# Performance work log

Hardware: AMD Instinct MI355X
Metric: run time of the kernel (lower is better)

The kernel has to match this reference:

```python
import jax, jax.numpy as jnp
import numpy as np
import math

NUM_HEADS = 16
HEAD_DIM = 128
HIDDEN = 2048
ROPE_THETA = 10000.0


def rotate_half(x):
    half = x.shape[-1] // 2
    return jnp.concatenate((-x[..., half:], x[..., :half]), axis=-1)


def rope_cos_sin(seq_len, dtype):
    # rotary_dim == head_dim (even)
    inv_freq = 1.0 / (ROPE_THETA ** (jnp.arange(0, HEAD_DIM, 2, dtype=jnp.float32) / HEAD_DIM))
    pos = jnp.arange(seq_len, dtype=jnp.float32)
    freqs = pos[:, None] * inv_freq[None, :]          # [S, HEAD_DIM/2]
    emb = jnp.concatenate((freqs, freqs), axis=-1)    # [S, HEAD_DIM]
    return jnp.cos(emb).astype(dtype), jnp.sin(emb).astype(dtype)


def setup_inputs() -> dict:
    key = jax.random.key(0)
    ks = jax.random.split(key, 5)
    B, S = 2, 2048
    scale = 1.0 / math.sqrt(HIDDEN)
    return {
        "hidden_states": jax.random.normal(ks[0], (B, S, HIDDEN), dtype=jnp.float32),
        "Wq": jax.random.normal(ks[1], (NUM_HEADS * HEAD_DIM, HIDDEN), dtype=jnp.float32) * scale,
        "Wk": jax.random.normal(ks[2], (NUM_HEADS * HEAD_DIM, HIDDEN), dtype=jnp.float32) * scale,
        "Wv": jax.random.normal(ks[3], (NUM_HEADS * HEAD_DIM, HIDDEN), dtype=jnp.float32) * scale,
        "Wo": jax.random.normal(ks[4], (HIDDEN, NUM_HEADS * HEAD_DIM), dtype=jnp.float32) * scale,
        "attention_mask": jnp.ones((B, S), dtype=bool),
    }


def reference(hidden_states, Wq, Wk, Wv, Wo, attention_mask):
    B, S, _ = hidden_states.shape
    # projections (Linear with weight [out, in]): y = x @ W.T
    def proj(W):
        y = jnp.einsum('bsh,oh->bso', hidden_states, W)
        return y.reshape(B, S, NUM_HEADS, HEAD_DIM).transpose(0, 2, 1, 3)  # [B,H,S,D]
    q, k, v = proj(Wq), proj(Wk), proj(Wv)

    cos, sin = rope_cos_sin(S, q.dtype)               # [S, D]
    cos = cos[None, None]                             # [1,1,S,D]
    sin = sin[None, None]
    q = q * cos + rotate_half(q) * sin
    k = k * cos + rotate_half(k) * sin

    scores = jnp.einsum('bhqd,bhkd->bhqk', q, k) / math.sqrt(HEAD_DIM)
    neg = jnp.finfo(scores.dtype).min
    causal = jnp.tril(jnp.ones((S, S), dtype=bool))   # past_len = 0
    scores = jnp.where(causal[None, None], scores, neg)
    key_mask = attention_mask[:, None, None, :]       # [B,1,1,S] bool
    scores = jnp.where(key_mask, scores, neg)

    attn = jax.nn.softmax(scores.astype(jnp.float32), axis=-1).astype(q.dtype)
    out = jnp.einsum('bhqk,bhkd->bhqd', attn, v)
    out = out.transpose(0, 2, 1, 3).reshape(B, S, NUM_HEADS * HEAD_DIM)
    return jnp.einsum('bso,ho->bsh', out, Wo)
```

## Files before the change

kernel.cpp:

```cpp
#include <hip/hip_runtime.h>
#include <stdint.h>

typedef unsigned short ushort_t;
typedef __attribute__((ext_vector_type(8))) __bf16 bf16x8;
typedef __attribute__((ext_vector_type(4))) float f32x4;

#define HIDDEN 2048
#define NHEADS 16
#define HDIM 128
#define SEQ 2048
#define BATCH 2
#define MROWS (BATCH*SEQ)

#define AS1 __attribute__((address_space(1)))
#define AS3 __attribute__((address_space(3)))

__device__ __forceinline__ ushort_t f2bf(float f) {
  uint32_t u = __float_as_uint(f);
  u += 0x7FFFu + ((u >> 16) & 1u);
  return (ushort_t)(u >> 16);
}
__device__ __forceinline__ float bf2f(ushort_t h) {
  return __uint_as_float((uint32_t)h << 16);
}

__device__ __forceinline__ f32x4 mfma16(bf16x8 a, bf16x8 b, f32x4 c) {
  return __builtin_amdgcn_mfma_f32_16x16x32_bf16(a, b, c, 0, 0, 0);
}

__global__ void cvt_kernel(const float* __restrict__ in, ushort_t* __restrict__ out, int n4) {
  int i = blockIdx.x * blockDim.x + threadIdx.x;
  if (i < n4) {
    float4 v = ((const float4*)in)[i];
    uint32_t lo = (uint32_t)f2bf(v.x) | ((uint32_t)f2bf(v.y) << 16);
    uint32_t hi = (uint32_t)f2bf(v.z) | ((uint32_t)f2bf(v.w) << 16);
    ((uint2*)out)[i] = make_uint2(lo, hi);
  }
}

__global__ void cvt4_kernel(const float* __restrict__ w0, const float* __restrict__ w1,
                            const float* __restrict__ w2, const float* __restrict__ w3,
                            ushort_t* __restrict__ o0, ushort_t* __restrict__ o1,
                            ushort_t* __restrict__ o2, ushort_t* __restrict__ o3) {
  int y = blockIdx.y;
  const float* in = (y == 0) ? w0 : (y == 1) ? w1 : (y == 2) ? w2 : w3;
  ushort_t* out = (y == 0) ? o0 : (y == 1) ? o1 : (y == 2) ? o2 : o3;
  int i = blockIdx.x * blockDim.x + threadIdx.x;
  float4 v = ((const float4*)in)[i];
  uint32_t lo = (uint32_t)f2bf(v.x) | ((uint32_t)f2bf(v.y) << 16);
  uint32_t hi = (uint32_t)f2bf(v.z) | ((uint32_t)f2bf(v.w) << 16);
  ((uint2*)out)[i] = make_uint2(lo, hi);
}

__device__ __forceinline__ void gemm128_core(const ushort_t* __restrict__ Ag,
                                             const ushort_t* __restrict__ Bg,
                                             ushort_t* As, ushort_t* Bs,
                                             f32x4 acc[4][4], int tid) {
  const int lane = tid & 63, wv = tid >> 6;
  const int r4 = lane >> 2;
  const int c8 = (((lane & 3) ^ ((r4 >> 1) & 3)) << 3);
  const int wm = (wv >> 1) * 64, wn = (wv & 1) * 64;
  const int mq = lane & 15, quad = lane >> 4;
  const int sw = (mq >> 1) & 3;

  auto stage = [&](int k0, int buf) {
#pragma unroll
    for (int cc = 0; cc < 2; ++cc) {
      int chunk = wv + cc * 4;
      const ushort_t* ga = Ag + (size_t)(chunk * 16 + r4) * HIDDEN + k0 + c8;
      const ushort_t* gb = Bg + (size_t)(chunk * 16 + r4) * HIDDEN + k0 + c8;
      __builtin_amdgcn_global_load_lds((AS1 void*)ga, (AS3 void*)(As + buf * 4096 + chunk * 512), 16, 0, 0);
      __builtin_amdgcn_global_load_lds((AS1 void*)gb, (AS3 void*)(Bs + buf * 4096 + chunk * 512), 16, 0, 0);
    }
  };

  stage(0, 0);
  __syncthreads();
#pragma unroll 1
  for (int k0 = 0; k0 < HIDDEN; k0 += 32) {
    const int cur = (k0 >> 5) & 1;
    if (k0 + 32 < HIDDEN) stage(k0 + 32, cur ^ 1);
    const ushort_t* A = As + cur * 4096;
    const ushort_t* B = Bs + cur * 4096;
    bf16x8 a[4], b[4];
#pragma unroll
    for (int i = 0; i < 4; ++i)
      a[i] = *(const bf16x8*)(A + (wm + i * 16 + mq) * 32 + ((quad ^ sw) << 3));
#pragma unroll
    for (int j = 0; j < 4; ++j)
      b[j] = *(const bf16x8*)(B + (wn + j * 16 + mq) * 32 + ((quad ^ sw) << 3));
#pragma unroll
    for (int i = 0; i < 4; ++i)
#pragma unroll
      for (int j = 0; j < 4; ++j)
        acc[i][j] = mfma16(a[i], b[j], acc[i][j]);
    __syncthreads();
  }
}

__global__ __launch_bounds__(256) void qkv_gemm(const ushort_t* __restrict__ X,
                                                const ushort_t* __restrict__ Wq,
                                                const ushort_t* __restrict__ Wk,
                                                const ushort_t* __restrict__ Wv,
                                                ushort_t* __restrict__ Q,
                                                ushort_t* __restrict__ K,
                                                ushort_t* __restrict__ Vt) {
  __shared__ __align__(16) ushort_t As[2][128 * 32];
  __shared__ __align__(16) ushort_t Bs[2][128 * 32];
  ushort_t* trans = &As[0][0];
  const int tid = threadIdx.x;
  const int lin = blockIdx.x;
  const int xcd = lin & 7, s = lin >> 3;
  const int by = xcd + 8 * (s % 6);
  const int bx = s / 6;
  const int m0 = bx * 128;
  const int nglob = by * 128;
  const int which = nglob >> 11;
  const int n0 = nglob & 2047;
  const ushort_t* W = (which == 0) ? Wq : ((which == 1) ? Wk : Wv);

  f32x4 acc[4][4];
  const f32x4 zf = {0.f, 0.f, 0.f, 0.f};
#pragma unroll
  for (int i = 0; i < 4; ++i)
#pragma unroll
    for (int j = 0; j < 4; ++j) acc[i][j] = zf;

  gemm128_core(X + (size_t)m0 * HIDDEN, W + (size_t)n0 * HIDDEN, &As[0][0], &Bs[0][0], acc, tid);

  const int lane = tid & 63, wv = tid >> 6;
  const int wm = (wv >> 1) * 64, wn = (wv & 1) * 64;
  const int mq = lane & 15, quad = lane >> 4;
  const int b = m0 >> 11, s0 = m0 & (SEQ - 1);
  const int h = n0 >> 7;

  if (which != 2) {
    ushort_t* dst = (which == 0) ? Q : K;
#pragma unroll
    for (int i = 0; i < 4; ++i)
#pragma unroll
      for (int j = 0; j < 4; ++j)
#pragma unroll
        for (int r = 0; r < 4; ++r) {
          int m = m0 + wm + i * 16 + quad * 4 + r;
          int o = n0 + wn + j * 16 + mq;
          int bb = m >> 11, sq = m & (SEQ - 1);
          int hh = o >> 7, d = o & (HDIM - 1);
          dst[((size_t)(bb * NHEADS + hh) * SEQ + sq) * HDIM + d] = f2bf(acc[i][j][r]);
        }
  } else {
#pragma unroll
    for (int p = 0; p < 2; ++p) {
      __syncthreads();
      if ((wv & 1) == p) {
#pragma unroll
        for (int i = 0; i < 4; ++i)
#pragma unroll
          for (int j = 0; j < 4; ++j)
#pragma unroll
            for (int r = 0; r < 4; ++r) {
              int m = wm + i * 16 + quad * 4 + r;
              int oo = j * 16 + mq;
              int mg = m >> 3;
              trans[oo * 128 + ((mg ^ (oo & 7)) * 8) + (m & 7)] = f2bf(acc[i][j][r]);
            }
      }
      __syncthreads();
#pragma unroll
      for (int it = 0; it < 4; ++it) {
        int oo = it * 16 + (tid >> 4);
        int g = tid & 15;
        uint4 v = *(const uint4*)(trans + oo * 128 + ((g ^ (oo & 7)) * 8));
        *(uint4*)(Vt + (((size_t)(b * NHEADS + h) * HDIM + (p * 64 + oo)) * SEQ + s0 + g * 8)) = v;
      }
    }
  }
}

__global__ void rope_kernel(ushort_t* __restrict__ Q, ushort_t* __restrict__ K) {
  int i = blockIdx.x * blockDim.x + threadIdx.x;
  int d = i & 63;
  int s = (i >> 6) & (SEQ - 1);
  int bh = i >> 17;
  size_t base = ((size_t)bh * SEQ + s) * HDIM;
  float inv = exp2f((float)d * -0.2076205059304601f);
  float ang = (float)s * inv;
  float sn, cs;
  sincosf(ang, &sn, &cs);
  const float scale = 0.08838834764831845f;
  float q0 = bf2f(Q[base + d]), q1 = bf2f(Q[base + d + 64]);
  Q[base + d]      = f2bf((q0 * cs - q1 * sn) * scale);
  Q[base + d + 64] = f2bf((q1 * cs + q0 * sn) * scale);
  float k0 = bf2f(K[base + d]), k1 = bf2f(K[base + d + 64]);
  K[base + d]      = f2bf(k0 * cs - k1 * sn);
  K[base + d + 64] = f2bf(k1 * cs + k0 * sn);
}

__global__ __launch_bounds__(256, 1) void flash_kernel(const ushort_t* __restrict__ Q,
                                                       const ushort_t* __restrict__ K,
                                                       const ushort_t* __restrict__ Vt,
                                                       ushort_t* __restrict__ Ao) {
  __shared__ __align__(16) ushort_t sK[2][64 * 128];
  __shared__ __align__(16) ushort_t sV[2][128 * 64];
  __shared__ __align__(16) ushort_t sP[128 * 64];
  ushort_t* sO = &sK[0][0];

  const int tid = threadIdx.x, lane = tid & 63, wv = tid >> 6;
  const int lq = lane & 15, quad = lane >> 4;
  const int lin = blockIdx.x;
  const int xcd = lin & 7, slot = lin >> 3;
  const int bh = xcd * 4 + (slot & 3);
  const int pair = slot >> 2;
  const ushort_t* Qb = Q + (size_t)bh * SEQ * HDIM;
  const ushort_t* Kb = K + (size_t)bh * SEQ * HDIM;
  const ushort_t* Vb = Vt + (size_t)bh * HDIM * SEQ;
  const int b = bh >> 4, h = bh & 15;

  auto stageK = [&](int j, ushort_t* dst) {
    int rr = lane >> 4, g = lane & 15;
#pragma unroll
    for (int t = 0; t < 4; ++t) {
      int chunk = wv * 4 + t;
      int row = chunk * 4 + rr;
      int gs = (g ^ (row & 7)) * 8;
      __builtin_amdgcn_global_load_lds((AS1 void*)(Kb + (size_t)(j * 64 + row) * HDIM + gs),
                                       (AS3 void*)(dst + chunk * 512), 16, 0, 0);
    }
  };
  auto stageV = [&](int j, ushort_t* dst) {
    int rr = lane >> 3, g = lane & 7;
#pragma unroll
    for (int t = 0; t < 4; ++t) {
      int chunk = wv * 4 + t;
      int row = chunk * 8 + rr;
      int gs = (g ^ (row & 7)) * 8;
      __builtin_amdgcn_global_load_lds((AS1 void*)(Vb + (size_t)row * SEQ + j * 64 + gs),
                                       (AS3 void*)(dst + chunk * 512), 16, 0, 0);
    }
  };

  const f32x4 zf = {0.f, 0.f, 0.f, 0.f};

#pragma unroll 1
  for (int phase = 0; phase < 2; ++phase) {
    const int T = phase ? (15 - pair) : pair;
    const int nsteps = 2 * T + 2;

    bf16x8 qf[2][4];
#pragma unroll
    for (int n = 0; n < 2; ++n)
#pragma unroll
      for (int kt = 0; kt < 4; ++kt)
        qf[n][kt] = *(const bf16x8*)(Qb + (size_t)(T * 128 + wv * 32 + n * 16 + lq) * HDIM +
                                     kt * 32 + quad * 8);

    float m_i[2] = {-1e30f, -1e30f}, l_i[2] = {0.f, 0.f};
    f32x4 oacc[8][2];
#pragma unroll
    for (int m = 0; m < 8; ++m)
#pragma unroll
      for (int n = 0; n < 2; ++n) oacc[m][n] = zf;

    __syncthreads();
    stageK(0, sK[0]);
    stageV(0, sV[0]);
    __syncthreads();

#pragma unroll 1
    for (int j = 0; j < nsteps; ++j) {
      const int cur = j & 1;
      if (j + 1 < nsteps) {
        stageK(j + 1, sK[cur ^ 1]);
        stageV(j + 1, sV[cur ^ 1]);
      }

      const ushort_t* sKc = sK[cur];
      f32x4 sacc[4][2];
#pragma unroll
      for (int m = 0; m < 4; ++m)
#pragma unroll
        for (int n = 0; n < 2; ++n) sacc[m][n] = zf;
#pragma unroll
      for (int kt = 0; kt < 4; ++kt) {
        bf16x8 kf[4];
#pragma unroll
        for (int m = 0; m < 4; ++m) {
          int row = m * 16 + lq;
          kf[m] = *(const bf16x8*)(sKc + row * 128 + (((kt * 4 + quad) ^ (row & 7)) * 8));
        }
#pragma unroll
        for (int m = 0; m < 4; ++m)
#pragma unroll
          for (int n = 0; n < 2; ++n)
            sacc[m][n] = mfma16(kf[m], qf[n][kt], sacc[m][n]);
      }

      const bool diag = (j >= 2 * T);
#pragma unroll
      for (int n = 0; n < 2; ++n) {
        const int qr = wv * 32 + n * 16 + lq;
        if (diag) {
          const int rowg = T * 128 + qr;
#pragma unroll
          for (int m = 0; m < 4; ++m)
#pragma unroll
            for (int r = 0; r < 4; ++r) {
              int key = j * 64 + m * 16 + quad * 4 + r;
              if (key > rowg) sacc[m][n][r] = -1e30f;
            }
        }
        float rm = -1e30f;
#pragma unroll
        for (int m = 0; m < 4; ++m)
#pragma unroll
          for (int r = 0; r < 4; ++r) rm = fmaxf(rm, sacc[m][n][r]);
        rm = fmaxf(rm, __shfl_xor(rm, 16, 64));
        rm = fmaxf(rm, __shfl_xor(rm, 32, 64));
        float mnew = fmaxf(m_i[n], rm);
        float alpha = __expf(m_i[n] - mnew);
        m_i[n] = mnew;
        float rs = 0.f;
#pragma unroll
        for (int m = 0; m < 4; ++m)
#pragma unroll
          for (int r = 0; r < 4; ++r) {
            float p = __expf(sacc[m][n][r] - mnew);
            sacc[m][n][r] = p;
            rs += p;
          }
        rs += __shfl_xor(rs, 16, 64);
        rs += __shfl_xor(rs, 32, 64);
        l_i[n] = l_i[n] * alpha + rs;
#pragma unroll
        for (int m = 0; m < 8; ++m)
#pragma unroll
          for (int r = 0; r < 4; ++r) oacc[m][n][r] *= alpha;
#pragma unroll
        for (int m = 0; m < 4; ++m) {
          uint32_t lo = (uint32_t)f2bf(sacc[m][n][0]) | ((uint32_t)f2bf(sacc[m][n][1]) << 16);
          uint32_t hi = (uint32_t)f2bf(sacc[m][n][2]) | ((uint32_t)f2bf(sacc[m][n][3]) << 16);
          int gw = m * 2 + (quad >> 1);
          *(uint2*)(sP + qr * 64 + ((gw ^ (qr & 7)) * 8) + (quad & 1) * 4) = make_uint2(lo, hi);
        }
      }

      const ushort_t* sVc = sV[cur];
#pragma unroll
      for (int kt = 0; kt < 2; ++kt) {
        bf16x8 pf[2];
#pragma unroll
        for (int n = 0; n < 2; ++n) {
          int qr = wv * 32 + n * 16 + lq;
          pf[n] = *(const bf16x8*)(sP + qr * 64 + (((kt * 4 + quad) ^ (qr & 7)) * 8));
        }
#pragma unroll
        for (int m = 0; m < 8; ++m) {
          int d = m * 16 + lq;
          bf16x8 vf = *(const bf16x8*)(sVc + d * 64 + (((kt * 4 + quad) ^ (d & 7)) * 8));
#pragma unroll
          for (int n = 0; n < 2; ++n)
            oacc[m][n] = mfma16(vf, pf[n], oacc[m][n]);
        }
      }

      __syncthreads();
    }

    float inv0 = 1.f / l_i[0], inv1 = 1.f / l_i[1];
#pragma unroll
    for (int n = 0; n < 2; ++n) {
      float inv = n ? inv1 : inv0;
      int qr = wv * 32 + n * 16 + lq;
#pragma unroll
      for (int m = 0; m < 8; ++m) {
        uint32_t lo = (uint32_t)f2bf(oacc[m][n][0] * inv) | ((uint32_t)f2bf(oacc[m][n][1] * inv) << 16);
        uint32_t hi = (uint32_t)f2bf(oacc[m][n][2] * inv) | ((uint32_t)f2bf(oacc[m][n][3] * inv) << 16);
        int gw = m * 2 + (quad >> 1);
        *(uint2*)(sO + qr * 128 + ((gw ^ (qr & 7)) * 8) + (quad & 1) * 4) = make_uint2(lo, hi);
      }
    }
    __syncthreads();
#pragma unroll
    for (int it = 0; it < 8; ++it) {
      int qr = it * 16 + (tid >> 4);
      int g = tid & 15;
      uint4 v = *(const uint4*)(sO + qr * 128 + ((g ^ (qr & 7)) * 8));
      *(uint4*)(Ao + ((size_t)(b * SEQ + T * 128 + qr)) * (NHEADS * HDIM) + h * HDIM + g * 8) = v;
    }
  }
}

__global__ __launch_bounds__(256) void out_gemm(const ushort_t* __restrict__ Ain,
                                                const ushort_t* __restrict__ Wo,
                                                float* __restrict__ Y) {
  __shared__ __align__(16) ushort_t As[2][128 * 32];
  __shared__ __align__(16) ushort_t Bs[2][128 * 32];
  const int tid = threadIdx.x;
  const int lin = blockIdx.x;
  const int xcd = lin & 7, s = lin >> 3;
  const int by = xcd + 8 * (s & 1);
  const int bx = s >> 1;
  const int m0 = bx * 128;
  const int n0 = by * 128;

  f32x4 acc[4][4];
  const f32x4 zf = {0.f, 0.f, 0.f, 0.f};
#pragma unroll
  for (int i = 0; i < 4; ++i)
#pragma unroll
    for (int j = 0; j < 4; ++j) acc[i][j] = zf;

  gemm128_core(Ain + (size_t)m0 * HIDDEN, Wo + (size_t)n0 * HIDDEN, &As[0][0], &Bs[0][0], acc, tid);

  const int lane = tid & 63, wv = tid >> 6;
  const int wm = (wv >> 1) * 64, wn = (wv & 1) * 64;
  const int mq = lane & 15, quad = lane >> 4;
#pragma unroll
  for (int i = 0; i < 4; ++i)
#pragma unroll
    for (int j = 0; j < 4; ++j)
#pragma unroll
      for (int r = 0; r < 4; ++r) {
        int m = m0 + wm + i * 16 + quad * 4 + r;
        int o = n0 + wn + j * 16 + mq;
        Y[(size_t)m * HIDDEN + o] = acc[i][j][r];
      }
}

extern "C" void kernel_launch(void* const* d_in, const int* in_sizes, int n_in,
                              void* d_out, int out_size, void* d_ws, size_t ws_size,
                              hipStream_t stream) {
  const float* hs = (const float*)d_in[0];
  const float* Wq = (const float*)d_in[1];
  const float* Wk = (const float*)d_in[2];
  const float* Wv = (const float*)d_in[3];
  const float* Wo = (const float*)d_in[4];
  float* out = (float*)d_out;

  ushort_t* ws  = (ushort_t*)d_ws;
  ushort_t* Xb  = ws;
  ushort_t* Wqb = Xb  + (size_t)MROWS * HIDDEN;
  ushort_t* Wkb = Wqb + (size_t)HIDDEN * HIDDEN;
  ushort_t* Wvb = Wkb + (size_t)HIDDEN * HIDDEN;
  ushort_t* Wob = Wvb + (size_t)HIDDEN * HIDDEN;
  ushort_t* Qb  = Wob + (size_t)HIDDEN * HIDDEN;
  ushort_t* Kb  = Qb  + (size_t)MROWS * HIDDEN;
  ushort_t* Vtb = Kb  + (size_t)MROWS * HIDDEN;
  ushort_t* Ao  = Vtb + (size_t)MROWS * HIDDEN;

  cvt_kernel<<<(MROWS * HIDDEN / 4) / 256, 256, 0, stream>>>(hs, Xb, MROWS * HIDDEN / 4);
  cvt4_kernel<<<dim3((HIDDEN * HIDDEN / 4) / 256, 4), 256, 0, stream>>>(
      Wq, Wk, Wv, Wo, Wqb, Wkb, Wvb, Wob);

  qkv_gemm<<<dim3(MROWS / 128 * 48), 256, 0, stream>>>(Xb, Wqb, Wkb, Wvb, Qb, Kb, Vtb);
  rope_kernel<<<(BATCH * NHEADS * SEQ * 64) / 256, 256, 0, stream>>>(Qb, Kb);
  flash_kernel<<<dim3(256), 256, 0, stream>>>(Qb, Kb, Vtb, Ao);
  out_gemm<<<dim3(512), 256, 0, stream>>>(Ao, Wob, out);
}
```

Measured before the change: 426.9 us.

## Rewrite QKV GEMM with 256x256 tiles, 8 waves, and direct-to-LDS pipelined loads

The QKV projection GEMM moves from 128x128 tiles on 256 threads to 256x256 tiles on 512 threads with a 64-wide K step. Global data goes straight into LDS via global_load_lds, and a phased schedule interleaves loads, barriers and MFMA with s_setprio. The aim is more reuse per tile, fewer global loads, and overlap of memory with compute. The cost is 128KB of LDS per block, higher register pressure, and only 384 blocks, which may leave CUs partly idle.

```diff
diff --git a/kernel.cpp b/kernel.cpp
--- a/kernel.cpp
+++ b/kernel.cpp
@@ -98,81 +98,177 @@
   }
 }
 
-__global__ __launch_bounds__(256) void qkv_gemm(const ushort_t* __restrict__ X,
-                                                const ushort_t* __restrict__ Wq,
-                                                const ushort_t* __restrict__ Wk,
-                                                const ushort_t* __restrict__ Wv,
-                                                ushort_t* __restrict__ Q,
-                                                ushort_t* __restrict__ K,
-                                                ushort_t* __restrict__ Vt) {
-  __shared__ __align__(16) ushort_t As[2][128 * 32];
-  __shared__ __align__(16) ushort_t Bs[2][128 * 32];
-  ushort_t* trans = &As[0][0];
-  const int tid = threadIdx.x;
+
+#define QKV_PHASE_MFMA(MH, NH, BB)                                                  \
+  __builtin_amdgcn_s_barrier();                                                     \
+  asm volatile("s_waitcnt lgkmcnt(0)" ::: "memory");                                \
+  __builtin_amdgcn_s_setprio(1);                                                    \
+  _Pragma("unroll") for (int f_ = 0; f_ < 4; ++f_)                                  \
+  _Pragma("unroll") for (int n_ = 0; n_ < 2; ++n_)                                  \
+  _Pragma("unroll") for (int kk_ = 0; kk_ < 2; ++kk_)                               \
+    acc[(MH)*4+f_][(NH)*2+n_] =                                                     \
+      mfma16(af[f_*2+kk_], BB[n_*2+kk_], acc[(MH)*4+f_][(NH)*2+n_]);                \
+  __builtin_amdgcn_s_setprio(0);
+
+#define QKV_TILE(CB, NB, KT)                                                        \
+  {                                                                                 \
+    const ushort_t* A_ = lds_q + (CB);                                              \
+    const ushort_t* B_ = lds_q + (CB) + 16384;                                      \
+    _Pragma("unroll") for (int u = 0; u < 8; ++u) af[u] = *(const bf16x8*)(A_ + aoff[u]); \
+    _Pragma("unroll") for (int u = 0; u < 4; ++u) b0r[u] = *(const bf16x8*)(B_ + boff[u]); \
+    stageA((KT), 0, (NB));                                                          \
+    QKV_PHASE_MFMA(0, 0, b0r)                                                       \
+    asm volatile("s_waitcnt vmcnt(4)" ::: "memory");                                \
+    __builtin_amdgcn_s_barrier();                                                   \
+    _Pragma("unroll") for (int u = 0; u < 4; ++u) b1r[u] = *(const bf16x8*)(B_ + 8192 + boff[u]); \
+    stageB((KT), 0, (NB));                                                          \
+    QKV_PHASE_MFMA(0, 1, b1r)                                                       \
+    asm volatile("s_waitcnt vmcnt(4)" ::: "memory");                                \
+    __builtin_amdgcn_s_barrier();                                                   \
+    _Pragma("unroll") for (int u = 0; u < 8; ++u) af[u] = *(const bf16x8*)(A_ + 8192 + aoff[u]); \
+    stageB((KT), 1, (NB));                                                          \
+    QKV_PHASE_MFMA(1, 1, b1r)                                                       \
+    __builtin_amdgcn_s_barrier();                                                   \
+    stageA((KT), 1, (NB));                                                          \
+    QKV_PHASE_MFMA(1, 0, b0r)                                                       \
+    asm volatile("s_waitcnt vmcnt(4)" ::: "memory");                                \
+    __builtin_amdgcn_s_barrier();                                                   \
+  }
+
+#define QKV_TAIL(CB)                                                                \
+  {                                                                                 \
+    const ushort_t* A_ = lds_q + (CB);                                              \
+    const ushort_t* B_ = lds_q + (CB) + 16384;                                      \
+    _Pragma("unroll") for (int u = 0; u < 8; ++u) af[u] = *(const bf16x8*)(A_ + aoff[u]); \
+    _Pragma("unroll") for (int u = 0; u < 4; ++u) b0r[u] = *(const bf16x8*)(B_ + boff[u]); \
+    QKV_PHASE_MFMA(0, 0, b0r)                                                       \
+    asm volatile("s_waitcnt vmcnt(2)" ::: "memory");                                \
+    __builtin_amdgcn_s_barrier();                                                   \
+    _Pragma("unroll") for (int u = 0; u < 4; ++u) b1r[u] = *(const bf16x8*)(B_ + 8192 + boff[u]); \
+    QKV_PHASE_MFMA(0, 1, b1r)                                                       \
+    asm volatile("s_waitcnt vmcnt(0)" ::: "memory");                                \
+    __builtin_amdgcn_s_barrier();                                                   \
+    _Pragma("unroll") for (int u = 0; u < 8; ++u) af[u] = *(const bf16x8*)(A_ + 8192 + aoff[u]); \
+    QKV_PHASE_MFMA(1, 1, b1r)                                                       \
+    __builtin_amdgcn_s_barrier();                                                   \
+    QKV_PHASE_MFMA(1, 0, b0r)                                                       \
+  }
+
+__global__ __launch_bounds__(512, 2) void qkv_gemm(const ushort_t* __restrict__ X,
+                                                   const ushort_t* __restrict__ Wq,
+                                                   const ushort_t* __restrict__ Wk,
+                                                   const ushort_t* __restrict__ Wv,
+                                                   ushort_t* __restrict__ Q,
+                                                   ushort_t* __restrict__ K,
+                                                   ushort_t* __restrict__ Vt) {
+  __shared__ __align__(16) ushort_t lds_q[65536];
+
+  const int tid = threadIdx.x, lane = tid & 63, wv = tid >> 6;
+  const int wr = wv >> 2, wc = wv & 3;
+  const int mq = lane & 15, quad = lane >> 4;
+  const int lr = lane >> 3;
+  const int csw = ((lane & 7) ^ (lr & 7)) * 8;
+
   const int lin = blockIdx.x;
   const int xcd = lin & 7, s = lin >> 3;
-  const int by = xcd + 8 * (s % 6);
-  const int bx = s / 6;
-  const int m0 = bx * 128;
-  const int nglob = by * 128;
+  const int by = xcd * 3 + (s % 3);
+  const int bx = s / 3;
+  const int m0 = bx * 256;
+  const int nglob = by * 256;
   const int which = nglob >> 11;
   const int n0 = nglob & 2047;
-  const ushort_t* W = (which == 0) ? Wq : ((which == 1) ? Wk : Wv);
-
-  f32x4 acc[4][4];
+  const ushort_t* Ag = X + (size_t)m0 * HIDDEN;
+  const ushort_t* Bg = ((which == 0) ? Wq : (which == 1) ? Wk : Wv) + (size_t)n0 * HIDDEN;
+
+  int aoff[8], boff[4];
+#pragma unroll
+  for (int f = 0; f < 4; ++f)
+#pragma unroll
+    for (int kk = 0; kk < 2; ++kk)
+      aoff[f * 2 + kk] = (f * 32 + wr * 16 + mq) * 64 + (((kk * 4 + quad) ^ (mq & 7)) * 8);
+#pragma unroll
+  for (int n = 0; n < 2; ++n)
+#pragma unroll
+    for (int kk = 0; kk < 2; ++kk)
+      boff[n * 2 + kk] = (n * 64 + wc * 16 + mq) * 64 + (((kk * 4 + quad) ^ (mq & 7)) * 8);
+
+  auto stageA = [&](int kt, int half, int nb) {
+#pragma unroll
+    for (int i = 0; i < 2; ++i) {
+      int seg = wv + i * 8;
+      const ushort_t* src = Ag + (size_t)(half * 128 + seg * 8 + lr) * HIDDEN + kt * 64 + csw;
+      __builtin_amdgcn_global_load_lds((AS1 void*)src,
+                                       (AS3 void*)(lds_q + nb + half * 8192 + seg * 512), 16, 0, 0);
+    }
+  };
+  auto stageB = [&](int kt, int half, int nb) {
+#pragma unroll
+    for (int i = 0; i < 2; ++i) {
+      int seg = wv + i * 8;
+      const ushort_t* src = Bg + (size_t)(half * 128 + seg * 8 + lr) * HIDDEN + kt * 64 + csw;
+      __builtin_amdgcn_global_load_lds((AS1 void*)src,
+                                       (AS3 void*)(lds_q + nb + 16384 + half * 8192 + seg * 512), 16, 0, 0);
+    }
+  };
+
+  f32x4 acc[8][4];
   const f32x4 zf = {0.f, 0.f, 0.f, 0.f};
 #pragma unroll
-  for (int i = 0; i < 4; ++i)
+  for (int i = 0; i < 8; ++i)
 #pragma unroll
     for (int j = 0; j < 4; ++j) acc[i][j] = zf;
 
-  gemm128_core(X + (size_t)m0 * HIDDEN, W + (size_t)n0 * HIDDEN, &As[0][0], &Bs[0][0], acc, tid);
-
-  const int lane = tid & 63, wv = tid >> 6;
-  const int wm = (wv >> 1) * 64, wn = (wv & 1) * 64;
-  const int mq = lane & 15, quad = lane >> 4;
-  const int b = m0 >> 11, s0 = m0 & (SEQ - 1);
-  const int h = n0 >> 7;
+  bf16x8 af[8], b0r[4], b1r[4];
+
+  stageA(0, 0, 0);
+  stageB(0, 0, 0);
+  stageB(0, 1, 0);
+  stageA(0, 1, 0);
+  __syncthreads();
+
+#pragma unroll 1
+  for (int tp = 0; tp < 15; ++tp) {
+    QKV_TILE(0, 32768, 2 * tp + 1)
+    QKV_TILE(32768, 0, 2 * tp + 2)
+  }
+  QKV_TILE(0, 32768, 31)
+  QKV_TAIL(32768)
 
   if (which != 2) {
     ushort_t* dst = (which == 0) ? Q : K;
 #pragma unroll
-    for (int i = 0; i < 4; ++i)
-#pragma unroll
-      for (int j = 0; j < 4; ++j)
+    for (int a = 0; a < 8; ++a)
+#pragma unroll
+      for (int c = 0; c < 4; ++c)
 #pragma unroll
         for (int r = 0; r < 4; ++r) {
-          int m = m0 + wm + i * 16 + quad * 4 + r;
-          int o = n0 + wn + j * 16 + mq;
-          int bb = m >> 11, sq = m & (SEQ - 1);
-          int hh = o >> 7, d = o & (HDIM - 1);
-          dst[((size_t)(bb * NHEADS + hh) * SEQ + sq) * HDIM + d] = f2bf(acc[i][j][r]);
+          int mrow = m0 + (a >> 2) * 128 + (a & 3) * 32 + wr * 16 + quad * 4 + r;
+          int ocol = n0 + (c >> 1) * 128 + (c & 1) * 64 + wc * 16 + mq;
+          int bb = mrow >> 11, sq = mrow & (SEQ - 1);
+          int hh = ocol >> 7, d = ocol & (HDIM - 1);
+          dst[((size_t)(bb * NHEADS + hh) * SEQ + sq) * HDIM + d] = f2bf(acc[a][c][r]);
         }
   } else {
-#pragma unroll
-    for (int p = 0; p < 2; ++p) {
-      __syncthreads();
-      if ((wv & 1) == p) {
-#pragma unroll
-        for (int i = 0; i < 4; ++i)
-#pragma unroll
-          for (int j = 0; j < 4; ++j)
-#pragma unroll
-            for (int r = 0; r < 4; ++r) {
-              int m = wm + i * 16 + quad * 4 + r;
-              int oo = j * 16 + mq;
-              int mg = m >> 3;
-              trans[oo * 128 + ((mg ^ (oo & 7)) * 8) + (m & 7)] = f2bf(acc[i][j][r]);
-            }
-      }
-      __syncthreads();
-#pragma unroll
-      for (int it = 0; it < 4; ++it) {
-        int oo = it * 16 + (tid >> 4);
-        int g = tid & 15;
-        uint4 v = *(const uint4*)(trans + oo * 128 + ((g ^ (oo & 7)) * 8));
-        *(uint4*)(Vt + (((size_t)(b * NHEADS + h) * HDIM + (p * 64 + oo)) * SEQ + s0 + g * 8)) = v;
-      }
+    __syncthreads();
+#pragma unroll
+    for (int a = 0; a < 8; ++a)
+#pragma unroll
+      for (int c4 = 0; c4 < 4; ++c4) {
+        int cc = (c4 >> 1) * 128 + (c4 & 1) * 64 + wc * 16 + mq;
+        int mb = (a >> 2) * 128 + (a & 3) * 32 + wr * 16 + quad * 4;
+        uint32_t lo = (uint32_t)f2bf(acc[a][c4][0]) | ((uint32_t)f2bf(acc[a][c4][1]) << 16);
+        uint32_t hi = (uint32_t)f2bf(acc[a][c4][2]) | ((uint32_t)f2bf(acc[a][c4][3]) << 16);
+        *(uint2*)(lds_q + cc * 256 + (mb ^ ((cc & 7) * 8))) = make_uint2(lo, hi);
+      }
+    __syncthreads();
+    const int bb = m0 >> 11, sq0 = m0 & (SEQ - 1);
+#pragma unroll
+    for (int it = 0; it < 16; ++it) {
+      int cc = it * 16 + (tid >> 5);
+      int sc = tid & 31;
+      uint4 v = *(const uint4*)(lds_q + cc * 256 + ((sc ^ (cc & 7)) * 8));
+      int hh = (n0 + cc) >> 7, d = (n0 + cc) & (HDIM - 1);
+      *(uint4*)(Vt + ((size_t)(bb * NHEADS + hh) * HDIM + d) * SEQ + sq0 + sc * 8) = v;
     }
   }
 }
@@ -452,7 +548,7 @@
   cvt4_kernel<<<dim3((HIDDEN * HIDDEN / 4) / 256, 4), 256, 0, stream>>>(
       Wq, Wk, Wv, Wo, Wqb, Wkb, Wvb, Wob);
 
-  qkv_gemm<<<dim3(MROWS / 128 * 48), 256, 0, stream>>>(Xb, Wqb, Wkb, Wvb, Qb, Kb, Vtb);
+  qkv_gemm<<<dim3(384), 512, 0, stream>>>(Xb, Wqb, Wkb, Wvb, Qb, Kb, Vtb);
   rope_kernel<<<(BATCH * NHEADS * SEQ * 64) / 256, 256, 0, stream>>>(Qb, Kb);
   flash_kernel<<<dim3(256), 256, 0, stream>>>(Qb, Kb, Vtb, Ao);
   out_gemm<<<dim3(512), 256, 0, stream>>>(Ao, Wob, out);
```

After: 403.3 us. -5.5%, faster.
